# Optimization experiments

Measured on AMD Instinct MI355X. Metric: run time of the kernel, lower is better.

The kernel has to match this reference:

```python
import jax, jax.numpy as jnp
import numpy as np

NUM_HEADS = 8
EPS = 1e-12  # torch F.normalize eps


def _l2norm(t):
    n = jnp.linalg.norm(t, axis=-1, keepdims=True)
    return t / jnp.maximum(n, EPS)


def setup_inputs() -> dict:
    key = jax.random.key(0)
    k1, k2, k3 = jax.random.split(key, 3)
    B, T, N, D = 16, 12, 1024, 128
    x = jax.random.normal(k1, (B, T, N, D), dtype=jnp.float32)
    # Linear(model_dim, 3*model_dim, bias=False): stored as (D, 3D) for x @ W
    W_qkv = jax.random.normal(k2, (D, 3 * D), dtype=jnp.float32) * (1.0 / np.sqrt(D))
    W_out = jax.random.normal(k3, (D, D), dtype=jnp.float32) * (1.0 / np.sqrt(D))
    b_out = jnp.zeros((D,), dtype=jnp.float32)
    return {"x": x, "W_qkv": W_qkv, "W_out": W_out, "b_out": b_out}


def reference(x, W_qkv, W_out, b_out):
    B, T, N, D = x.shape
    H = NUM_HEADS
    hd = D // H
    qkv = x @ W_qkv                                  # (B,T,N,3D)
    q, k, v = jnp.split(qkv, 3, axis=-1)
    # split heads + flatten (B,T) -> b = B*T, matching torch stack/flatten
    qs = _l2norm(q.reshape(B * T, N, H, hd))          # (b,N,H,m)
    ks = _l2norm(k.reshape(B * T, N, H, hd))
    vs = v.reshape(B * T, N, H, hd)
    # linear attention: running kv sum + normalizer
    kvs = jnp.einsum('blhm,blhd->bhmd', ks, vs)       # (b,H,m,d)
    attn_num = jnp.einsum('bnhm,bhmd->bnhd', qs, kvs) + N * vs
    ks_sum = jnp.sum(ks, axis=1)                      # (b,H,m)
    normalizer = jnp.einsum('bnhm,bhm->bnh', qs, ks_sum)[..., None] + N
    out = attn_num / normalizer                       # (b,N,H,d)
    out = out.reshape(B, T, N, D)
    return out @ W_out + b_out
```

## Files before the change

kernel.cpp:

```cpp
#include <hip/hip_runtime.h>

#define NBATCH 192
#define SEQ    1024
#define DIM    128
#define NH     8
#define EPS    1e-12f

typedef short bf16x8 __attribute__((ext_vector_type(8)));
typedef float f32x4  __attribute__((ext_vector_type(4)));

#define KVS_F  393216
#define ZERO_F 417792

static __device__ __forceinline__ unsigned short f2bf(float f) {
    unsigned u = __builtin_bit_cast(unsigned, f);
    u += 0x7fff + ((u >> 16) & 1);
    return (unsigned short)(u >> 16);
}

template <int CTRL>
static __device__ __forceinline__ float dpp_add(float v) {
    int j = __builtin_amdgcn_mov_dpp(__builtin_bit_cast(int, v), CTRL, 0xf, 0xf, false);
    return v + __builtin_bit_cast(float, j);
}
static __device__ __forceinline__ float r16sum(float v) {
    v = dpp_add<0xB1>(v);
    v = dpp_add<0x4E>(v);
    v = dpp_add<0x141>(v);
    v = dpp_add<0x140>(v);
    return v;
}

static __device__ __forceinline__ int strip_addr(int row, int el) {
    return row * 32 + ((((el >> 3) ^ (row & 3)) << 3) | (el & 7));
}

static __device__ __forceinline__ uint2 pack4(float a, float b, float c, float d) {
    uint2 r;
    r.x = (unsigned)f2bf(a) | ((unsigned)f2bf(b) << 16);
    r.y = (unsigned)f2bf(c) | ((unsigned)f2bf(d) << 16);
    return r;
}

static __device__ __forceinline__ bf16x8 cvt8(float4 a, float4 b) {
    bf16x8 r;
    r[0] = (short)f2bf(a.x); r[1] = (short)f2bf(a.y); r[2] = (short)f2bf(a.z); r[3] = (short)f2bf(a.w);
    r[4] = (short)f2bf(b.x); r[5] = (short)f2bf(b.y); r[6] = (short)f2bf(b.z); r[7] = (short)f2bf(b.w);
    return r;
}

static __device__ __forceinline__ bf16x8 gfrag(const unsigned short* __restrict__ wT,
                                               int ct, int ks, int lane) {
    return *reinterpret_cast<const bf16x8*>(wT + ((ct * 4 + ks) * 64 + lane) * 8);
}

__global__ __launch_bounds__(256) void k0_prep(const float* __restrict__ Wqkv,
                                               const float* __restrict__ Wout,
                                               unsigned short* __restrict__ wsWT) {
    int i = blockIdx.x * 256 + threadIdx.x;
    int which = i >> 14, e = i & 16383;
    int j = e & 7, f = e >> 3;
    int n15 = f & 15, q = (f >> 4) & 3, ks = (f >> 6) & 3, ct = f >> 8;
    int k = ks * 32 + q * 8 + j, n = ct * 16 + n15;
    float v = (which < 3) ? Wqkv[k * 384 + which * 128 + n] : Wout[k * 128 + n];
    wsWT[i] = f2bf(v);
}

__global__ __launch_bounds__(512, 6) void k1_kv(const float* __restrict__ x,
                                                const unsigned short* __restrict__ wsWT,
                                                float* __restrict__ kvs_ws,
                                                float* __restrict__ kssum_ws) {
    __shared__ float kvsagg[2048];
    __shared__ unsigned short strips[8192];
    int t = threadIdx.x, w = t >> 6, lane = t & 63, q = lane >> 4, n15 = lane & 15;
    int b = blockIdx.x >> 2, seg = blockIdx.x & 3;
    const unsigned short* wkT = wsWT + 16384;
    const unsigned short* wvT = wsWT + 32768;
    unsigned short* knS = strips + w * 1024;
    unsigned short* vS  = knS + 512;

#pragma unroll
    for (int i = 0; i < 4; ++i) kvsagg[i * 512 + t] = 0.0f;

    bf16x8 ah[2][4];
#pragma unroll
    for (int rs = 0; rs < 2; ++rs) {
        int row = seg * 256 + w * 32 + rs * 16 + n15;
        const float* xr = x + (size_t)(b * SEQ + row) * DIM;
#pragma unroll
        for (int ks = 0; ks < 4; ++ks) {
            float4 p0 = *reinterpret_cast<const float4*>(xr + ks * 32 + q * 8);
            float4 p1 = *reinterpret_cast<const float4*>(xr + ks * 32 + q * 8 + 4);
            ah[rs][ks] = cvt8(p0, p1);
        }
    }
    __syncthreads();

#pragma unroll 1
    for (int ct = 0; ct < 8; ++ct) {
        f32x4 ka[2] = {(f32x4){0,0,0,0}, (f32x4){0,0,0,0}};
        f32x4 va[2] = {(f32x4){0,0,0,0}, (f32x4){0,0,0,0}};
#pragma unroll
        for (int ks = 0; ks < 4; ++ks) {
            bf16x8 kb = gfrag(wkT, ct, ks, lane);
            bf16x8 vb = gfrag(wvT, ct, ks, lane);
#pragma unroll
            for (int rs = 0; rs < 2; ++rs) {
                ka[rs] = __builtin_amdgcn_mfma_f32_16x16x32_bf16(ah[rs][ks], kb, ka[rs], 0, 0, 0);
                va[rs] = __builtin_amdgcn_mfma_f32_16x16x32_bf16(ah[rs][ks], vb, va[rs], 0, 0, 0);
            }
        }
        float ksum = 0.f;
#pragma unroll
        for (int rs = 0; rs < 2; ++rs) {
            float kn[4];
#pragma unroll
            for (int r = 0; r < 4; ++r) {
                float val = ka[rs][r];
                float ssq = r16sum(val * val);
                float di  = 1.0f / fmaxf(sqrtf(ssq), EPS);
                kn[r] = val * di;
                ksum += kn[r];
            }
            *reinterpret_cast<uint2*>(knS + strip_addr(n15, rs * 16 + q * 4)) =
                pack4(kn[0], kn[1], kn[2], kn[3]);
            *reinterpret_cast<uint2*>(vS + strip_addr(n15, rs * 16 + q * 4)) =
                pack4(va[rs][0], va[rs][1], va[rs][2], va[rs][3]);
        }
        bf16x8 aK = *reinterpret_cast<const bf16x8*>(knS + strip_addr(n15, q * 8));
        bf16x8 bV = *reinterpret_cast<const bf16x8*>(vS + strip_addr(n15, q * 8));
        f32x4 kacc = __builtin_amdgcn_mfma_f32_16x16x32_bf16(aK, bV, (f32x4){0,0,0,0}, 0, 0, 0);
#pragma unroll
        for (int r = 0; r < 4; ++r)
            atomicAdd(&kvsagg[ct * 256 + (q * 4 + r) * 16 + n15], kacc[r]);
        float s = ksum;
        s += __shfl_xor(s, 16); s += __shfl_xor(s, 32);
        if (lane < 16) atomicAdd(&kssum_ws[b * 128 + ct * 16 + n15], s);
    }

    __syncthreads();
#pragma unroll
    for (int i = 0; i < 4; ++i) {
        int el = i * 512 + t;
        atomicAdd(&kvs_ws[b * 2048 + el], kvsagg[el]);
    }
}

__global__ __launch_bounds__(512, 6) void k2_out(const float* __restrict__ x,
                                                 const unsigned short* __restrict__ wsWT,
                                                 const float* __restrict__ kvs_ws,
                                                 const float* __restrict__ kssum_ws,
                                                 const float* __restrict__ bout,
                                                 float* __restrict__ out) {
    __shared__ unsigned short lds[24576];
    unsigned short* kvsT   = lds;
    unsigned short* strips = lds + 4096;
    unsigned short* tile   = lds + 8192;
    int t = threadIdx.x, w = t >> 6, lane = t & 63, q = lane >> 4, n15 = lane & 15;
    int b = blockIdx.x >> 2, seg = blockIdx.x & 3, rowbase = seg * 256;
    const unsigned short* wqT = wsWT;
    const unsigned short* wvT = wsWT + 32768;
    const unsigned short* woT = wsWT + 49152;

    {
        int row = t >> 2, part = t & 3, h = row >> 4, d = row & 15;
        unsigned es[8];
#pragma unroll
        for (int j = 0; j < 8; j += 2) {
            int m0 = part * 8 + j;
            unsigned lo = (m0     < 16) ? f2bf(kvs_ws[b * 2048 + h * 256 + m0 * 16 + d])      : 0;
            unsigned hi = (m0 + 1 < 16) ? f2bf(kvs_ws[b * 2048 + h * 256 + (m0 + 1) * 16 + d]) : 0;
            es[j] = lo | (hi << 16);
        }
        uint4 v = {es[0], es[2], es[4], es[6]};
        *reinterpret_cast<uint4*>(kvsT + row * 32 + ((part ^ (row & 3)) << 3)) = v;
    }

    bf16x8 ah[2][4];
#pragma unroll
    for (int rs = 0; rs < 2; ++rs) {
        int row = rowbase + w * 32 + rs * 16 + n15;
        const float* xr = x + (size_t)(b * SEQ + row) * DIM;
#pragma unroll
        for (int ks = 0; ks < 4; ++ks) {
            float4 p0 = *reinterpret_cast<const float4*>(xr + ks * 32 + q * 8);
            float4 p1 = *reinterpret_cast<const float4*>(xr + ks * 32 + q * 8 + 4);
            ah[rs][ks] = cvt8(p0, p1);
        }
    }

    unsigned short* myS = strips + w * 512;
    unsigned short* tw  = tile + w * 2048;
    {
        uint2 z = {0, 0};
        *reinterpret_cast<uint2*>(myS + strip_addr(n15, 16 + q * 4)) = z;
    }
    __syncthreads();

#pragma unroll
    for (int rs = 0; rs < 2; ++rs) {
#pragma unroll 1
        for (int h = 0; h < 8; ++h) {
            float kssh = kssum_ws[b * 128 + h * 16 + n15];
            f32x4 qa = (f32x4){0,0,0,0};
            f32x4 va = (f32x4){0,0,0,0};
#pragma unroll
            for (int ks = 0; ks < 4; ++ks) {
                bf16x8 qb = gfrag(wqT, h, ks, lane);
                bf16x8 vb = gfrag(wvT, h, ks, lane);
                qa = __builtin_amdgcn_mfma_f32_16x16x32_bf16(ah[rs][ks], qb, qa, 0, 0, 0);
                va = __builtin_amdgcn_mfma_f32_16x16x32_bf16(ah[rs][ks], vb, va, 0, 0, 0);
            }
            float pv[4];
#pragma unroll
            for (int r = 0; r < 4; ++r) {
                float val = qa[r];
                float ssq = r16sum(val * val);
                float tt  = r16sum(val * kssh);
                float di  = 1.0f / fmaxf(sqrtf(ssq), EPS);
                float inv = 1.0f / (tt * di + (float)SEQ);
                pv[r] = val * di * inv;
                va[r] *= (float)SEQ * inv;
            }
#pragma unroll
            for (int r = 0; r < 4; ++r)
                myS[strip_addr(q * 4 + r, n15)] = f2bf(pv[r]);
            bf16x8 aq = *reinterpret_cast<const bf16x8*>(myS + strip_addr(n15, q * 8));
            bf16x8 bk = *reinterpret_cast<const bf16x8*>(kvsT + strip_addr(h * 16 + n15, q * 8));
            va = __builtin_amdgcn_mfma_f32_16x16x32_bf16(aq, bk, va, 0, 0, 0);
#pragma unroll
            for (int r = 0; r < 4; ++r) {
                int rt = q * 4 + r;
                int colg = h * 2 + (n15 >> 3);
                tw[rt * 128 + (((colg ^ rt) << 3) | (n15 & 7))] = f2bf(va[r]);
            }
        }

        bf16x8 ap[4];
#pragma unroll
        for (int ks = 0; ks < 4; ++ks)
            ap[ks] = *reinterpret_cast<const bf16x8*>(
                tw + n15 * 128 + ((((ks << 2) + q) ^ n15) << 3));
#pragma unroll 1
        for (int ct = 0; ct < 8; ++ct) {
            f32x4 oa = (f32x4){0,0,0,0};
#pragma unroll
            for (int ks = 0; ks < 4; ++ks) {
                bf16x8 bb = gfrag(woT, ct, ks, lane);
                oa = __builtin_amdgcn_mfma_f32_16x16x32_bf16(ap[ks], bb, oa, 0, 0, 0);
            }
            float bo = bout[ct * 16 + n15];
#pragma unroll
            for (int r = 0; r < 4; ++r) {
                int row = rowbase + w * 32 + rs * 16 + q * 4 + r;
                out[(size_t)(b * SEQ + row) * DIM + ct * 16 + n15] = oa[r] + bo;
            }
        }
    }
}

extern "C" void kernel_launch(void* const* d_in, const int* in_sizes, int n_in,
                              void* d_out, int out_size, void* d_ws, size_t ws_size,
                              hipStream_t stream) {
    const float* x    = (const float*)d_in[0];
    const float* Wqkv = (const float*)d_in[1];
    const float* Wout = (const float*)d_in[2];
    const float* bout = (const float*)d_in[3];
    float* out = (float*)d_out;

    float* kvs_ws   = (float*)d_ws;
    float* kssum_ws = kvs_ws + KVS_F;
    unsigned short* wsWT = (unsigned short*)((char*)d_ws + (size_t)ZERO_F * 4);

    hipMemsetAsync(d_ws, 0, (size_t)ZERO_F * 4, stream);
    k0_prep<<<dim3(256), dim3(256), 0, stream>>>(Wqkv, Wout, wsWT);
    k1_kv<<<dim3(768), dim3(512), 0, stream>>>(x, wsWT, kvs_ws, kssum_ws);
    k2_out<<<dim3(768), dim3(512), 0, stream>>>(x, wsWT, kvs_ws, kssum_ws, bout, out);
}
```

Measured before the change: 331.3 us.

## Cache bf16 x between kernels, fold memset into prep, replace LDS atomics

k1 now writes its bf16-converted x fragments to workspace so k2 reads half the bytes instead of reloading fp32 x, when the workspace is large enough. The memset is folded into the prep kernel as extra blocks. The LDS atomic accumulation of per-wave kv products is replaced by per-wave buffers summed at the end, and conversions use packed hardware bf16 intrinsics. In exchange it adds extra global writes in k1, a larger LDS footprint and a lower occupancy hint.

```diff
diff --git a/kernel.cpp b/kernel.cpp
--- a/kernel.cpp
+++ b/kernel.cpp
@@ -1,4 +1,5 @@
 #include <hip/hip_runtime.h>
+#include <hip/hip_bf16.h>
 
 #define NBATCH 192
 #define SEQ    1024
@@ -9,13 +10,30 @@
 typedef short bf16x8 __attribute__((ext_vector_type(8)));
 typedef float f32x4  __attribute__((ext_vector_type(4)));
 
-#define KVS_F  393216
-#define ZERO_F 417792
+#define KVS_F   393216
+#define ZERO_F  417792
+#define WSWT_OFF ((size_t)ZERO_F * 4)
+#define XB_OFF   (WSWT_OFF + 131072)
+#define XB_SHPB  32768
+#define WS_NEED  (XB_OFF + (size_t)768 * XB_SHPB * 2)
 
 static __device__ __forceinline__ unsigned short f2bf(float f) {
     unsigned u = __builtin_bit_cast(unsigned, f);
     u += 0x7fff + ((u >> 16) & 1);
     return (unsigned short)(u >> 16);
+}
+
+static __device__ __forceinline__ unsigned pk2(float a, float b) {
+    __hip_bfloat162 h = __float22bfloat162_rn(make_float2(a, b));
+    unsigned r;
+    __builtin_memcpy(&r, &h, 4);
+    return r;
+}
+static __device__ __forceinline__ unsigned short bf1(float a) {
+    __hip_bfloat16 h = __float2bfloat16(a);
+    unsigned short r;
+    __builtin_memcpy(&r, &h, 2);
+    return r;
 }
 
 template <int CTRL>
@@ -37,16 +55,16 @@
 
 static __device__ __forceinline__ uint2 pack4(float a, float b, float c, float d) {
     uint2 r;
-    r.x = (unsigned)f2bf(a) | ((unsigned)f2bf(b) << 16);
-    r.y = (unsigned)f2bf(c) | ((unsigned)f2bf(d) << 16);
+    r.x = pk2(a, b);
+    r.y = pk2(c, d);
     return r;
 }
 
 static __device__ __forceinline__ bf16x8 cvt8(float4 a, float4 b) {
-    bf16x8 r;
-    r[0] = (short)f2bf(a.x); r[1] = (short)f2bf(a.y); r[2] = (short)f2bf(a.z); r[3] = (short)f2bf(a.w);
-    r[4] = (short)f2bf(b.x); r[5] = (short)f2bf(b.y); r[6] = (short)f2bf(b.z); r[7] = (short)f2bf(b.w);
-    return r;
+    uint4 u;
+    u.x = pk2(a.x, a.y); u.y = pk2(a.z, a.w);
+    u.z = pk2(b.x, b.y); u.w = pk2(b.z, b.w);
+    return __builtin_bit_cast(bf16x8, u);
 }
 
 static __device__ __forceinline__ bf16x8 gfrag(const unsigned short* __restrict__ wT,
@@ -56,8 +74,11 @@
 
 __global__ __launch_bounds__(256) void k0_prep(const float* __restrict__ Wqkv,
                                                const float* __restrict__ Wout,
+                                               float* __restrict__ zero_p,
                                                unsigned short* __restrict__ wsWT) {
-    int i = blockIdx.x * 256 + threadIdx.x;
+    int bid = blockIdx.x, t = threadIdx.x;
+    if (bid < 1632) { zero_p[bid * 256 + t] = 0.0f; return; }
+    int i = (bid - 1632) * 256 + t;
     int which = i >> 14, e = i & 16383;
     int j = e & 7, f = e >> 3;
     int n15 = f & 15, q = (f >> 4) & 3, ks = (f >> 6) & 3, ct = f >> 8;
@@ -66,11 +87,13 @@
     wsWT[i] = f2bf(v);
 }
 
-__global__ __launch_bounds__(512, 6) void k1_kv(const float* __restrict__ x,
+__global__ __launch_bounds__(512, 4) void k1_kv(const float* __restrict__ x,
                                                 const unsigned short* __restrict__ wsWT,
                                                 float* __restrict__ kvs_ws,
-                                                float* __restrict__ kssum_ws) {
-    __shared__ float kvsagg[2048];
+                                                float* __restrict__ kssum_ws,
+                                                unsigned short* __restrict__ xb,
+                                                int writeXb) {
+    __shared__ float redf[16384];
     __shared__ unsigned short strips[8192];
     int t = threadIdx.x, w = t >> 6, lane = t & 63, q = lane >> 4, n15 = lane & 15;
     int b = blockIdx.x >> 2, seg = blockIdx.x & 3;
@@ -79,9 +102,6 @@
     unsigned short* knS = strips + w * 1024;
     unsigned short* vS  = knS + 512;
 
-#pragma unroll
-    for (int i = 0; i < 4; ++i) kvsagg[i * 512 + t] = 0.0f;
-
     bf16x8 ah[2][4];
 #pragma unroll
     for (int rs = 0; rs < 2; ++rs) {
@@ -94,7 +114,15 @@
             ah[rs][ks] = cvt8(p0, p1);
         }
     }
-    __syncthreads();
+    if (writeXb) {
+        unsigned short* xo = xb + (size_t)blockIdx.x * XB_SHPB + t * 8;
+#pragma unroll
+        for (int rs = 0; rs < 2; ++rs)
+#pragma unroll
+            for (int ks = 0; ks < 4; ++ks)
+                *reinterpret_cast<uint4*>(xo + (rs * 4 + ks) * 4096) =
+                    __builtin_bit_cast(uint4, ah[rs][ks]);
+    }
 
 #pragma unroll 1
     for (int ct = 0; ct < 8; ++ct) {
@@ -132,7 +160,7 @@
         f32x4 kacc = __builtin_amdgcn_mfma_f32_16x16x32_bf16(aK, bV, (f32x4){0,0,0,0}, 0, 0, 0);
 #pragma unroll
         for (int r = 0; r < 4; ++r)
-            atomicAdd(&kvsagg[ct * 256 + (q * 4 + r) * 16 + n15], kacc[r]);
+            redf[w * 2048 + ct * 256 + (q * 4 + r) * 16 + n15] = kacc[r];
         float s = ksum;
         s += __shfl_xor(s, 16); s += __shfl_xor(s, 32);
         if (lane < 16) atomicAdd(&kssum_ws[b * 128 + ct * 16 + n15], s);
@@ -142,16 +170,21 @@
 #pragma unroll
     for (int i = 0; i < 4; ++i) {
         int el = i * 512 + t;
-        atomicAdd(&kvs_ws[b * 2048 + el], kvsagg[el]);
-    }
-}
-
-__global__ __launch_bounds__(512, 6) void k2_out(const float* __restrict__ x,
+        float s = 0.f;
+#pragma unroll
+        for (int ww = 0; ww < 8; ++ww) s += redf[ww * 2048 + el];
+        atomicAdd(&kvs_ws[b * 2048 + el], s);
+    }
+}
+
+template <int XB>
+__global__ __launch_bounds__(512, 4) void k2_out(const float* __restrict__ x,
                                                  const unsigned short* __restrict__ wsWT,
                                                  const float* __restrict__ kvs_ws,
                                                  const float* __restrict__ kssum_ws,
                                                  const float* __restrict__ bout,
-                                                 float* __restrict__ out) {
+                                                 float* __restrict__ out,
+                                                 const unsigned short* __restrict__ xb) {
     __shared__ unsigned short lds[24576];
     unsigned short* kvsT   = lds;
     unsigned short* strips = lds + 4096;
@@ -168,24 +201,33 @@
 #pragma unroll
         for (int j = 0; j < 8; j += 2) {
             int m0 = part * 8 + j;
-            unsigned lo = (m0     < 16) ? f2bf(kvs_ws[b * 2048 + h * 256 + m0 * 16 + d])      : 0;
-            unsigned hi = (m0 + 1 < 16) ? f2bf(kvs_ws[b * 2048 + h * 256 + (m0 + 1) * 16 + d]) : 0;
-            es[j] = lo | (hi << 16);
+            float lo = (m0     < 16) ? kvs_ws[b * 2048 + h * 256 + m0 * 16 + d]       : 0.f;
+            float hi = (m0 + 1 < 16) ? kvs_ws[b * 2048 + h * 256 + (m0 + 1) * 16 + d] : 0.f;
+            es[j] = pk2(lo, hi);
         }
         uint4 v = {es[0], es[2], es[4], es[6]};
         *reinterpret_cast<uint4*>(kvsT + row * 32 + ((part ^ (row & 3)) << 3)) = v;
     }
 
     bf16x8 ah[2][4];
-#pragma unroll
-    for (int rs = 0; rs < 2; ++rs) {
-        int row = rowbase + w * 32 + rs * 16 + n15;
-        const float* xr = x + (size_t)(b * SEQ + row) * DIM;
-#pragma unroll
-        for (int ks = 0; ks < 4; ++ks) {
-            float4 p0 = *reinterpret_cast<const float4*>(xr + ks * 32 + q * 8);
-            float4 p1 = *reinterpret_cast<const float4*>(xr + ks * 32 + q * 8 + 4);
-            ah[rs][ks] = cvt8(p0, p1);
+    if (XB) {
+        const unsigned short* xi = xb + (size_t)blockIdx.x * XB_SHPB + t * 8;
+#pragma unroll
+        for (int rs = 0; rs < 2; ++rs)
+#pragma unroll
+            for (int ks = 0; ks < 4; ++ks)
+                ah[rs][ks] = *reinterpret_cast<const bf16x8*>(xi + (rs * 4 + ks) * 4096);
+    } else {
+#pragma unroll
+        for (int rs = 0; rs < 2; ++rs) {
+            int row = rowbase + w * 32 + rs * 16 + n15;
+            const float* xr = x + (size_t)(b * SEQ + row) * DIM;
+#pragma unroll
+            for (int ks = 0; ks < 4; ++ks) {
+                float4 p0 = *reinterpret_cast<const float4*>(xr + ks * 32 + q * 8);
+                float4 p1 = *reinterpret_cast<const float4*>(xr + ks * 32 + q * 8 + 4);
+                ah[rs][ks] = cvt8(p0, p1);
+            }
         }
     }
 
@@ -224,7 +266,7 @@
             }
 #pragma unroll
             for (int r = 0; r < 4; ++r)
-                myS[strip_addr(q * 4 + r, n15)] = f2bf(pv[r]);
+                myS[strip_addr(q * 4 + r, n15)] = bf1(pv[r]);
             bf16x8 aq = *reinterpret_cast<const bf16x8*>(myS + strip_addr(n15, q * 8));
             bf16x8 bk = *reinterpret_cast<const bf16x8*>(kvsT + strip_addr(h * 16 + n15, q * 8));
             va = __builtin_amdgcn_mfma_f32_16x16x32_bf16(aq, bk, va, 0, 0, 0);
@@ -232,7 +274,7 @@
             for (int r = 0; r < 4; ++r) {
                 int rt = q * 4 + r;
                 int colg = h * 2 + (n15 >> 3);
-                tw[rt * 128 + (((colg ^ rt) << 3) | (n15 & 7))] = f2bf(va[r]);
+                tw[rt * 128 + (((colg ^ rt) << 3) | (n15 & 7))] = bf1(va[r]);
             }
         }
 
@@ -270,10 +312,14 @@
 
     float* kvs_ws   = (float*)d_ws;
     float* kssum_ws = kvs_ws + KVS_F;
-    unsigned short* wsWT = (unsigned short*)((char*)d_ws + (size_t)ZERO_F * 4);
-
-    hipMemsetAsync(d_ws, 0, (size_t)ZERO_F * 4, stream);
-    k0_prep<<<dim3(256), dim3(256), 0, stream>>>(Wqkv, Wout, wsWT);
-    k1_kv<<<dim3(768), dim3(512), 0, stream>>>(x, wsWT, kvs_ws, kssum_ws);
-    k2_out<<<dim3(768), dim3(512), 0, stream>>>(x, wsWT, kvs_ws, kssum_ws, bout, out);
-}
+    unsigned short* wsWT = (unsigned short*)((char*)d_ws + WSWT_OFF);
+    unsigned short* xb   = (unsigned short*)((char*)d_ws + XB_OFF);
+    int use_xb = (ws_size >= WS_NEED) ? 1 : 0;
+
+    k0_prep<<<dim3(1888), dim3(256), 0, stream>>>(Wqkv, Wout, kvs_ws, wsWT);
+    k1_kv<<<dim3(768), dim3(512), 0, stream>>>(x, wsWT, kvs_ws, kssum_ws, xb, use_xb);
+    if (use_xb)
+        k2_out<1><<<dim3(768), dim3(512), 0, stream>>>(x, wsWT, kvs_ws, kssum_ws, bout, out, xb);
+    else
+        k2_out<0><<<dim3(768), dim3(512), 0, stream>>>(x, wsWT, kvs_ws, kssum_ws, bout, out, xb);
+}
```

Result: faster. 284.7 us (-14.0%).
